# Kernel optimization log

Measured on AMD Instinct MI355X. Metric: run time of the kernel, lower is better.

Reference implementation:

```python
import jax, jax.numpy as jnp
import numpy as np

B, L, DIM = 2, 2048, 2048
H, KV, HD = 32, 8, 64
N_REP = H // KV


def setup_inputs() -> dict:
    key = jax.random.key(0)
    ks = jax.random.split(key, 6)
    std = DIM ** -0.5
    std_o = (H * HD) ** -0.5 / np.sqrt(2 * 24)
    x = jax.random.normal(ks[0], (B, L, DIM), dtype=jnp.float32)
    # freqs_cis packs (cos, sin), each [L, head_dim//2]
    pos = jnp.arange(L, dtype=jnp.float32)[:, None]
    inv = 1.0 / (10000.0 ** (jnp.arange(0, HD, 2, dtype=jnp.float32) / HD))
    ang = pos * inv[None, :]
    freqs_cis = jnp.stack([jnp.cos(ang), jnp.sin(ang)], axis=0)
    wq = jax.random.normal(ks[1], (H * HD, DIM), dtype=jnp.float32) * std
    wk = jax.random.normal(ks[2], (KV * HD, DIM), dtype=jnp.float32) * std
    wv = jax.random.normal(ks[3], (KV * HD, DIM), dtype=jnp.float32) * std
    wo = jax.random.normal(ks[4], (DIM, H * HD), dtype=jnp.float32) * std_o
    return {"x": x, "freqs_cis": freqs_cis, "wq": wq, "wk": wk, "wv": wv, "wo": wo}


def _rope(t, cos, sin):
    # t: [B, L, h, HD]; interleaved (real, imag) pairs in last dim
    tr = t.reshape(*t.shape[:-1], HD // 2, 2)
    out_r = tr[..., 0] * cos - tr[..., 1] * sin
    out_i = tr[..., 0] * sin + tr[..., 1] * cos
    return jnp.stack([out_r, out_i], axis=-1).reshape(t.shape)


def reference(x, freqs_cis, wq, wk, wv, wo):
    Bb, Ll, _ = x.shape
    xq = (x @ wq.T).reshape(Bb, Ll, H, HD)
    xk = (x @ wk.T).reshape(Bb, Ll, KV, HD)
    xv = (x @ wv.T).reshape(Bb, Ll, KV, HD)
    cos = freqs_cis[0].reshape(1, Ll, 1, HD // 2)
    sin = freqs_cis[1].reshape(1, Ll, 1, HD // 2)
    xq = _rope(xq, cos, sin)
    xk = _rope(xk, cos, sin)
    # GQA: repeat_interleave kv heads to n_heads
    xk = jnp.repeat(xk, N_REP, axis=2)
    xv = jnp.repeat(xv, N_REP, axis=2)
    scale = 1.0 / jnp.sqrt(jnp.asarray(HD, x.dtype))
    scores = jnp.einsum('bihd,bjhd->bhij', xq, xk) * scale
    causal = jnp.tril(jnp.ones((Ll, Ll), dtype=bool))
    scores = jnp.where(causal[None, None], scores, jnp.finfo(scores.dtype).min)
    attn = jax.nn.softmax(scores, axis=-1)
    out = jnp.einsum('bhij,bjhd->bihd', attn, xv).reshape(Bb, Ll, H * HD)
    return out @ wo.T
```

## Files before the change

### kernel.cpp

```cpp
#include <hip/hip_runtime.h>
#include <stdint.h>

typedef __bf16 bf16;
typedef __attribute__((ext_vector_type(8))) __bf16 bf16x8;
typedef __attribute__((ext_vector_type(4))) __bf16 bf16x4;
typedef __attribute__((ext_vector_type(8))) short short8v;
typedef __attribute__((ext_vector_type(4))) short short4v;
typedef __attribute__((ext_vector_type(4))) float f32x4;

static constexpr int Bn = 2, Ln = 2048, DIMn = 2048, Hn = 32, KVn = 8, HDn = 64;
static constexpr int TS = 3072;

#if defined(__has_builtin)
#if __has_builtin(__builtin_amdgcn_exp2f)
#define EXP2(x) __builtin_amdgcn_exp2f(x)
#endif
#endif
#ifndef EXP2
#define EXP2(x) exp2f(x)
#endif

#define TO_LDS(p) ((__attribute__((address_space(3))) uint32_t*)(uintptr_t)(p))
#define TO_GLB(p) ((const __attribute__((address_space(1))) uint32_t*)(uintptr_t)(p))

__global__ void cast_all(const float* __restrict__ x, const float* __restrict__ wq,
                         const float* __restrict__ wk, const float* __restrict__ wv,
                         const float* __restrict__ wo, bf16* __restrict__ xb,
                         bf16* __restrict__ wqkvb, bf16* __restrict__ wob) {
    size_t i = (size_t)(blockIdx.x * blockDim.x + threadIdx.x) * 4;
    const float* src;
    bf16* dst;
    if (i < 8388608) {
        src = x + i; dst = xb + i;
    } else if (i < 8388608 + 6291456) {
        size_t j = i - 8388608;
        dst = wqkvb + j;
        if (j < 4194304)      src = wq + j;
        else if (j < 5242880) src = wk + (j - 4194304);
        else                  src = wv + (j - 5242880);
    } else {
        size_t j = i - 14680064;
        src = wo + j; dst = wob + j;
    }
    float4 v = *(const float4*)src;
    bf16 o[4] = {(bf16)v.x, (bf16)v.y, (bf16)v.z, (bf16)v.w};
    *(uint64_t*)dst = *(uint64_t*)o;
}

__global__ void rope_k(bf16* __restrict__ qkv, const float* __restrict__ fc) {
    int idx = blockIdx.x * blockDim.x + threadIdx.x;
    int i   = idx & 31;
    int kvh = (idx >> 5) & 7;
    int bl  = idx >> 8;
    int l   = bl & (Ln - 1);
    size_t base = (size_t)bl * TS + 2048 + kvh * 64 + 2 * i;
    float cr = fc[l * 32 + i];
    float sr = fc[65536 + l * 32 + i];
    float x0 = (float)qkv[base], x1 = (float)qkv[base + 1];
    qkv[base]     = (bf16)(x0 * cr - x1 * sr);
    qkv[base + 1] = (bf16)(x0 * sr + x1 * cr);
}

static __device__ __forceinline__ void barrier_f() {
    asm volatile("" ::: "memory");
    __builtin_amdgcn_s_barrier();
    asm volatile("" ::: "memory");
}

template <int N>
static __device__ __forceinline__ void waitcnt_vm() {
    if constexpr (N == 0) asm volatile("s_waitcnt vmcnt(0)" ::: "memory");
    else if constexpr (N == 6) asm volatile("s_waitcnt vmcnt(6)" ::: "memory");
    else if constexpr (N == 7) asm volatile("s_waitcnt vmcnt(7)" ::: "memory");
    else static_assert(N == 0 || N == 6 || N == 7, "add vmcnt literal");
}

template <int BM, int BN, bool OUT_BF16>
__global__ __launch_bounds__(512, 2) void gemm256(const bf16* __restrict__ A,
                                                  const bf16* __restrict__ Bm,
                                                  void* __restrict__ C,
                                                  int M, int N, int K) {
    (void)M;
    constexpr int MI = BM / 32;
    constexpr int NI = BN / 64;
    constexpr int AJ = BM / 64, BJ = BN / 64, LPT = AJ + BJ;
    __shared__ bf16 sA[2][BM * 64];
    __shared__ bf16 sB[2][BN * 64];
    const int t    = threadIdx.x;
    const int wave = t >> 6, lane = t & 63;
    const int q4 = lane >> 4, l16 = lane & 15;
    const int wm = wave >> 2, wn = wave & 3;
    const int r8l = lane >> 3;
    const int csw = ((lane & 7) ^ r8l) * 8;

    const size_t bm = (size_t)blockIdx.y * BM, bn = (size_t)blockIdx.x * BN;
    const bf16* pa = A  + (bm + (size_t)(wave * 8 + r8l)) * K + csw;
    const bf16* pb = Bm + (bn + (size_t)(wave * 8 + r8l)) * K + csw;
    const int NT = K >> 6;

#define STGA(buf, kt)                                                                          \
    _Pragma("unroll") for (int j = 0; j < AJ; ++j)                                             \
        __builtin_amdgcn_global_load_lds(TO_GLB(pa + (size_t)j * 64 * K + (size_t)(kt) * 64),  \
                                         TO_LDS(&sA[buf][(j * 64 + wave * 8) * 64]), 16, 0, 0)
#define STGB(buf, kt)                                                                          \
    _Pragma("unroll") for (int j = 0; j < BJ; ++j)                                             \
        __builtin_amdgcn_global_load_lds(TO_GLB(pb + (size_t)j * 64 * K + (size_t)(kt) * 64),  \
                                         TO_LDS(&sB[buf][(j * 64 + wave * 8) * 64]), 16, 0, 0)

    STGA(0, 0); STGB(0, 0);
    STGA(1, 1); STGB(1, 1);
    waitcnt_vm<LPT>();
    __builtin_amdgcn_s_barrier();
    asm volatile("" ::: "memory");

    f32x4 acc[MI][NI] = {};
    bf16x8 af[MI][2], bfr[NI][2];

    for (int k = 0; k < NT; ++k) {
        const int c = k & 1;
        const bf16* la = &sA[c][0];
        const bf16* lb = &sB[c][0];
        const int sw = (l16 & 7);

#pragma unroll
        for (int mi = 0; mi < MI / 2; ++mi)
#pragma unroll
            for (int kk = 0; kk < 2; ++kk)
                af[mi][kk] = *(const bf16x8*)(la + (wm * (BM / 2) + mi * 16 + l16) * 64 +
                                              ((kk * 4 + q4) ^ sw) * 8);
#pragma unroll
        for (int ni = 0; ni < NI; ++ni)
#pragma unroll
            for (int kk = 0; kk < 2; ++kk)
                bfr[ni][kk] = *(const bf16x8*)(lb + (wn * (BN / 4) + ni * 16 + l16) * 64 +
                                               ((kk * 4 + q4) ^ sw) * 8);
#pragma unroll
        for (int mi = MI / 2; mi < MI; ++mi)
#pragma unroll
            for (int kk = 0; kk < 2; ++kk)
                af[mi][kk] = *(const bf16x8*)(la + (wm * (BM / 2) + mi * 16 + l16) * 64 +
                                              ((kk * 4 + q4) ^ sw) * 8);

        __builtin_amdgcn_s_setprio(1);
#pragma unroll
        for (int mi = 0; mi < MI; ++mi)
#pragma unroll
            for (int ni = 0; ni < NI; ++ni)
#pragma unroll
                for (int kk = 0; kk < 2; ++kk)
                    acc[mi][ni] = __builtin_amdgcn_mfma_f32_16x16x32_bf16(
                        af[mi][kk], bfr[ni][kk], acc[mi][ni], 0, 0, 0);
        __builtin_amdgcn_s_setprio(0);

        barrier_f();

        if (k + 2 < NT) {
            STGA(c, k + 2);
            STGB(c, k + 2);
            waitcnt_vm<LPT>();
        } else if (k == NT - 2) {
            waitcnt_vm<0>();
        }
        barrier_f();
    }
#undef STGA
#undef STGB

#pragma unroll
    for (int mi = 0; mi < MI; ++mi)
#pragma unroll
        for (int ni = 0; ni < NI; ++ni)
#pragma unroll
            for (int r = 0; r < 4; ++r) {
                size_t row = bm + wm * (BM / 2) + mi * 16 + q4 * 4 + r;
                size_t col = bn + wn * (BN / 4) + ni * 16 + l16;
                if (OUT_BF16)
                    ((bf16*)C)[row * (size_t)N + col] = (bf16)acc[mi][ni][r];
                else
                    ((float*)C)[row * (size_t)N + col] = acc[mi][ni][r];
            }
}

__global__ __launch_bounds__(256, 2) void attn_kernel(const bf16* __restrict__ QKV,
                                                      const float* __restrict__ fc,
                                                      bf16* __restrict__ O) {
    constexpr int LDK = 72;
    __shared__ bf16 sK[64 * LDK];
    __shared__ bf16 sV[64 * LDK];
    const int t    = threadIdx.x;
    const int wave = t >> 6, lane = t & 63;
    const int q4 = lane >> 4, l16 = lane & 15;
    const int hidx = wave & 1, qh = wave >> 1;
    const int L = blockIdx.x;
    const int qtile = 31 - (L >> 5);
    const int inner = L & 31;
    const int b = inner & 1, kvh = (inner >> 1) & 7, hp = (inner >> 4) & 1;
    const int h = kvh * 4 + hp * 2 + hidx;
    constexpr float SC = 0.125f * 1.44269504088896340736f;

    const bf16* kb = QKV + (size_t)(b * Ln) * TS + 2048 + kvh * 64;
    const bf16* vb = kb + 512;
    const int krow = t >> 3;
    const int kc8  = (t & 7) * 8;
    const int kp2  = (t & 31) * 2;
    const int vh8  = (t >> 5) * 8;

    bf16x8 qf[2][2];
#pragma unroll
    for (int g2 = 0; g2 < 2; ++g2) {
        int ql = qtile * 64 + (qh * 2 + g2) * 16 + l16;
        const bf16* qp = QKV + (size_t)(b * Ln + ql) * TS + h * 64;
#pragma unroll
        for (int hc = 0; hc < 2; ++hc) {
            bf16x8 raw = *(const bf16x8*)(qp + hc * 32 + q4 * 8);
            float4 c4 = *(const float4*)(fc + ql * 32 + hc * 16 + q4 * 4);
            float4 s4 = *(const float4*)(fc + 65536 + ql * 32 + hc * 16 + q4 * 4);
            bf16x8 o;
#pragma unroll
            for (int m = 0; m < 4; ++m) {
                float cr = ((const float*)&c4)[m], sr = ((const float*)&s4)[m];
                float x0 = (float)raw[2 * m], x1 = (float)raw[2 * m + 1];
                o[2 * m]     = (bf16)((x0 * cr - x1 * sr) * SC);
                o[2 * m + 1] = (bf16)((x0 * sr + x1 * cr) * SC);
            }
            qf[g2][hc] = o;
        }
    }

    f32x4 o_acc[2][4] = {};
    float l_r[2] = {0.f, 0.f};

    bf16x8 kreg[2], vrA, vrB;
#pragma unroll
    for (int p = 0; p < 2; ++p)
        kreg[p] = *(const bf16x8*)(kb + (size_t)(p * 32 + krow) * TS + kc8);
    vrA = *(const bf16x8*)(vb + (size_t)kp2 * TS + vh8);
    vrB = *(const bf16x8*)(vb + (size_t)(kp2 + 1) * TS + vh8);

    for (int kt = 0; kt <= qtile; ++kt) {
#pragma unroll
        for (int p = 0; p < 2; ++p)
            *(float4*)(&sK[(p * 32 + krow) * LDK + kc8]) = *(float4*)&kreg[p];
        {
            short8v sa = __builtin_bit_cast(short8v, vrA);
            short8v sb = __builtin_bit_cast(short8v, vrB);
#pragma unroll
            for (int j = 0; j < 8; ++j) {
                uint32_t d = (uint32_t)(uint16_t)sa[j] |
                             ((uint32_t)(uint16_t)sb[j] << 16);
                *(uint32_t*)(&sV[(vh8 + j) * LDK + kp2]) = d;
            }
        }
        __syncthreads();

        if (kt < qtile) {
#pragma unroll
            for (int p = 0; p < 2; ++p)
                kreg[p] = *(const bf16x8*)(kb + (size_t)((kt + 1) * 64 + p * 32 + krow) * TS + kc8);
            vrA = *(const bf16x8*)(vb + (size_t)((kt + 1) * 64 + kp2) * TS + vh8);
            vrB = *(const bf16x8*)(vb + (size_t)((kt + 1) * 64 + kp2 + 1) * TS + vh8);
        }

        bf16x8 kf[4][2];
#pragma unroll
        for (int c = 0; c < 4; ++c)
#pragma unroll
            for (int hc = 0; hc < 2; ++hc)
                kf[c][hc] = *(const bf16x8*)(&sK[(c * 16 + l16) * LDK + hc * 32 + q4 * 8]);
        short4v vf[4][4];
#pragma unroll
        for (int nc = 0; nc < 4; ++nc)
#pragma unroll
            for (int c = 0; c < 4; ++c)
                vf[nc][c] = *(const short4v*)(&sV[(nc * 16 + l16) * LDK + c * 16 + q4 * 4]);

        const bool diag = (kt == qtile);
#pragma unroll
        for (int g2 = 0; g2 < 2; ++g2) {
            f32x4 s[4];
            __builtin_amdgcn_s_setprio(1);
#pragma unroll
            for (int c = 0; c < 4; ++c) {
                f32x4 a = {};
                a = __builtin_amdgcn_mfma_f32_16x16x32_bf16(kf[c][0], qf[g2][0], a, 0, 0, 0);
                a = __builtin_amdgcn_mfma_f32_16x16x32_bf16(kf[c][1], qf[g2][1], a, 0, 0, 0);
                s[c] = a;
            }
            __builtin_amdgcn_s_setprio(0);
            int qrow = qtile * 64 + (qh * 2 + g2) * 16 + l16;
            float lsum = 0.f;
            short4v pb4[4];
            if (diag) {
#pragma unroll
                for (int c = 0; c < 4; ++c) {
                    float pc[4];
#pragma unroll
                    for (int r = 0; r < 4; ++r) {
                        float p = EXP2(s[c][r] - 12.f);
                        if (kt * 64 + c * 16 + q4 * 4 + r > qrow) p = 0.f;
                        pc[r] = p;
                        bf16 ph = (bf16)p;
                        pb4[c][r] = *(const short*)&ph;
                    }
                    lsum += (pc[0] + pc[1]) + (pc[2] + pc[3]);
                }
            } else {
#pragma unroll
                for (int c = 0; c < 4; ++c) {
                    float pc[4];
#pragma unroll
                    for (int r = 0; r < 4; ++r) {
                        float p = EXP2(s[c][r] - 12.f);
                        pc[r] = p;
                        bf16 ph = (bf16)p;
                        pb4[c][r] = *(const short*)&ph;
                    }
                    lsum += (pc[0] + pc[1]) + (pc[2] + pc[3]);
                }
            }
            l_r[g2] += lsum;
            __builtin_amdgcn_s_setprio(1);
#pragma unroll
            for (int nc = 0; nc < 4; ++nc)
#pragma unroll
                for (int c = 0; c < 4; ++c)
                    o_acc[g2][nc] = __builtin_amdgcn_mfma_f32_16x16x16bf16_1k(
                        vf[nc][c], pb4[c], o_acc[g2][nc], 0, 0, 0);
            __builtin_amdgcn_s_setprio(0);
        }
        __syncthreads();
    }

#pragma unroll
    for (int g2 = 0; g2 < 2; ++g2) {
        float l = l_r[g2];
        l += __shfl_xor(l, 16, 64);
        l += __shfl_xor(l, 32, 64);
        float inv = 1.f / l;
        int qrow = qtile * 64 + (qh * 2 + g2) * 16 + l16;
        bf16* op = O + (size_t)(b * Ln + qrow) * (Hn * HDn) + h * 64;
#pragma unroll
        for (int nc = 0; nc < 4; ++nc) {
            bf16x4 o;
#pragma unroll
            for (int r = 0; r < 4; ++r) o[r] = (bf16)(o_acc[g2][nc][r] * inv);
            *(bf16x4*)(op + nc * 16 + q4 * 4) = o;
        }
    }
}

extern "C" void kernel_launch(void* const* d_in, const int* in_sizes, int n_in,
                              void* d_out, int out_size, void* d_ws, size_t ws_size,
                              hipStream_t stream) {
    const float* x  = (const float*)d_in[0];
    const float* fc = (const float*)d_in[1];
    const float* wq = (const float*)d_in[2];
    const float* wk = (const float*)d_in[3];
    const float* wv = (const float*)d_in[4];
    const float* wo = (const float*)d_in[5];
    float* out = (float*)d_out;

    const size_t T = (size_t)Bn * Ln;
    char* p = (char*)d_ws;
    bf16* xb    = (bf16*)p; p += T * DIMn * 2;
    bf16* wqkvb = (bf16*)p; p += (size_t)TS * DIMn * 2;
    bf16* wob   = (bf16*)p; p += (size_t)DIMn * Hn * HDn * 2;
    bf16* qkv   = (bf16*)p; p += T * TS * 2;
    bf16* ao    = (bf16*)p; p += T * Hn * HDn * 2;

    cast_all<<<dim3(18432), dim3(256), 0, stream>>>(x, wq, wk, wv, wo, xb, wqkvb, wob);

    gemm256<256, 192, true><<<dim3(TS / 192, 4096 / 256), dim3(512), 0, stream>>>(
        xb, wqkvb, qkv, 4096, TS, 2048);

    rope_k<<<dim3(4096), dim3(256), 0, stream>>>(qkv, fc);

    attn_kernel<<<dim3(1024), dim3(256), 0, stream>>>(qkv, fc, ao);

    gemm256<128, 256, false><<<dim3(2048 / 256, 4096 / 128), dim3(512), 0, stream>>>(
        ao, wob, out, 4096, 2048, 2048);
}
```

Baseline: 276.1 us.

## Split GEMM main loop into four MFMA quadrants interleaved with LDS reads and staging

```diff
diff --git a/kernel.cpp b/kernel.cpp
--- a/kernel.cpp
+++ b/kernel.cpp
@@ -76,13 +76,15 @@
 }
 
 template <int BM, int BN, bool OUT_BF16>
-__global__ __launch_bounds__(512, 2) void gemm256(const bf16* __restrict__ A,
+__global__ __launch_bounds__(512, 1) void gemm256(const bf16* __restrict__ A,
                                                   const bf16* __restrict__ Bm,
                                                   void* __restrict__ C,
                                                   int M, int N, int K) {
     (void)M;
     constexpr int MI = BM / 32;
     constexpr int NI = BN / 64;
+    constexpr int MLO = MI / 2, MHI = MI - MLO;
+    constexpr int NLO = NI / 2, NHI = NI - NLO;
     constexpr int AJ = BM / 64, BJ = BN / 64, LPT = AJ + BJ;
     __shared__ bf16 sA[2][BM * 64];
     __shared__ bf16 sB[2][BN * 64];
@@ -107,6 +109,22 @@
         __builtin_amdgcn_global_load_lds(TO_GLB(pb + (size_t)j * 64 * K + (size_t)(kt) * 64),  \
                                          TO_LDS(&sB[buf][(j * 64 + wave * 8) * 64]), 16, 0, 0)
 
+#define RDA(mi_)                                                                               \
+    _Pragma("unroll") for (int kk = 0; kk < 2; ++kk)                                           \
+        af[mi_][kk] = *(const bf16x8*)(la + (wm * (BM / 2) + (mi_) * 16 + l16) * 64 +          \
+                                       ((kk * 4 + q4) ^ sw) * 8)
+#define RDB(ni_)                                                                               \
+    _Pragma("unroll") for (int kk = 0; kk < 2; ++kk)                                           \
+        bfr[ni_][kk] = *(const bf16x8*)(lb + (wn * (BN / 4) + (ni_) * 16 + l16) * 64 +         \
+                                        ((kk * 4 + q4) ^ sw) * 8)
+
+#define MMQ(m0, mc, n0, nc2)                                                                   \
+    _Pragma("unroll") for (int mi = 0; mi < (mc); ++mi)                                        \
+    _Pragma("unroll") for (int ni = 0; ni < (nc2); ++ni)                                       \
+    _Pragma("unroll") for (int kk = 0; kk < 2; ++kk)                                           \
+        acc[(m0) + mi][(n0) + ni] = __builtin_amdgcn_mfma_f32_16x16x32_bf16(                   \
+            af[(m0) + mi][kk], bfr[(n0) + ni][kk], acc[(m0) + mi][(n0) + ni], 0, 0, 0)
+
     STGA(0, 0); STGB(0, 0);
     STGA(1, 1); STGB(1, 1);
     waitcnt_vm<LPT>();
@@ -123,48 +141,49 @@
         const int sw = (l16 & 7);
 
 #pragma unroll
-        for (int mi = 0; mi < MI / 2; ++mi)
-#pragma unroll
-            for (int kk = 0; kk < 2; ++kk)
-                af[mi][kk] = *(const bf16x8*)(la + (wm * (BM / 2) + mi * 16 + l16) * 64 +
-                                              ((kk * 4 + q4) ^ sw) * 8);
-#pragma unroll
-        for (int ni = 0; ni < NI; ++ni)
-#pragma unroll
-            for (int kk = 0; kk < 2; ++kk)
-                bfr[ni][kk] = *(const bf16x8*)(lb + (wn * (BN / 4) + ni * 16 + l16) * 64 +
-                                               ((kk * 4 + q4) ^ sw) * 8);
-#pragma unroll
-        for (int mi = MI / 2; mi < MI; ++mi)
-#pragma unroll
-            for (int kk = 0; kk < 2; ++kk)
-                af[mi][kk] = *(const bf16x8*)(la + (wm * (BM / 2) + mi * 16 + l16) * 64 +
-                                              ((kk * 4 + q4) ^ sw) * 8);
-
+        for (int mi = 0; mi < MLO; ++mi) { RDA(mi); }
+#pragma unroll
+        for (int ni = 0; ni < NLO; ++ni) { RDB(ni); }
+        barrier_f();
         __builtin_amdgcn_s_setprio(1);
-#pragma unroll
-        for (int mi = 0; mi < MI; ++mi)
-#pragma unroll
-            for (int ni = 0; ni < NI; ++ni)
-#pragma unroll
-                for (int kk = 0; kk < 2; ++kk)
-                    acc[mi][ni] = __builtin_amdgcn_mfma_f32_16x16x32_bf16(
-                        af[mi][kk], bfr[ni][kk], acc[mi][ni], 0, 0, 0);
+        MMQ(0, MLO, 0, NLO);
         __builtin_amdgcn_s_setprio(0);
-
+        barrier_f();
+
+#pragma unroll
+        for (int mi = MLO; mi < MI; ++mi) { RDA(mi); }
+#pragma unroll
+        for (int ni = NLO; ni < NI; ++ni) { RDB(ni); }
+        barrier_f();
+        __builtin_amdgcn_s_setprio(1);
+        MMQ(MLO, MHI, NLO, NHI);
+        __builtin_amdgcn_s_setprio(0);
+        barrier_f();
+
+        if (k + 2 < NT) { STGA(c, k + 2); }
+        barrier_f();
+        __builtin_amdgcn_s_setprio(1);
+        MMQ(MLO, MHI, 0, NLO);
+        __builtin_amdgcn_s_setprio(0);
         barrier_f();
 
         if (k + 2 < NT) {
-            STGA(c, k + 2);
             STGB(c, k + 2);
             waitcnt_vm<LPT>();
         } else if (k == NT - 2) {
             waitcnt_vm<0>();
         }
         barrier_f();
+        __builtin_amdgcn_s_setprio(1);
+        MMQ(0, MLO, NLO, NHI);
+        __builtin_amdgcn_s_setprio(0);
+        barrier_f();
     }
 #undef STGA
 #undef STGB
+#undef RDA
+#undef RDB
+#undef MMQ
 
 #pragma unroll
     for (int mi = 0; mi < MI; ++mi)
```

Measured after the change: 279.2 us. Within noise of the previous version (+1.1%).
